# Optimization experiments

Hardware: AMD Instinct MI355X
Metric: run time of the kernel (lower is better)

The kernel has to match this reference:

```python
import jax, jax.numpy as jnp
import numpy as np

B, H, S, DK = 2, 8, 4096, 64


def setup_inputs() -> dict:
    key = jax.random.key(0)
    kq, kk, kv = jax.random.split(key, 3)
    queries = jax.random.normal(kq, (B, H, S, DK), dtype=jnp.float32)
    keys = jax.random.normal(kk, (B, H, S, DK), dtype=jnp.float32)
    values = jax.random.normal(kv, (B, H, S, DK), dtype=jnp.float32)
    # causal mask: 1.0 where attention is disallowed (strictly upper triangle)
    mask = jnp.triu(jnp.ones((S, S), dtype=jnp.float32), k=1)
    return {"queries": queries, "keys": keys, "values": values, "d_k": DK, "mask": mask}


def reference(queries, keys, values, d_k, mask):
    # scores: [B, H, S, S]
    scale = 1.0 / jnp.sqrt(jnp.float32(d_k))
    scores = jnp.einsum("bhqd,bhkd->bhqk", queries, keys) * scale
    if mask is not None:
        scores = scores + (-1e9) * mask  # broadcast [S,S] over [B,H,S,S]
    weights = jax.nn.softmax(scores, axis=-1)
    return jnp.einsum("bhqk,bhkd->bhqd", weights, values)
```

## Files before the change

### kernel.cpp

```cpp
#include <hip/hip_runtime.h>

typedef __bf16 bf16x8 __attribute__((ext_vector_type(8)));
typedef unsigned short u16x8 __attribute__((ext_vector_type(8)));
typedef unsigned short u16x4 __attribute__((ext_vector_type(4)));
typedef float f32x4 __attribute__((ext_vector_type(4)));

#define MFMA16(a, b, c) __builtin_amdgcn_mfma_f32_16x16x32_bf16((a), (b), (c), 0, 0, 0)

constexpr int SEQ  = 4096;
constexpr int DH   = 64;
constexpr int BH   = 16;
constexpr int LSTR = 72;
constexpr float SCALE_LOG2E = 0.125f * 1.44269504088896f;

__device__ __forceinline__ unsigned short f2bf(float f) {
  unsigned int u = __float_as_uint(f);
  u += 0x7fffu + ((u >> 16) & 1u);
  return (unsigned short)(u >> 16);
}

__global__ __launch_bounds__(256)
void prep_9990093930993(const float* __restrict__ K, const float* __restrict__ V,
                        unsigned short* __restrict__ Kb, unsigned short* __restrict__ Vtb) {
  const int tile = blockIdx.x, bh = blockIdx.y, tid = threadIdx.x;

  {
    const int row = tid >> 2;
    const int c0  = (tid & 3) * 16;
    const float* kr = K + (((long)bh * SEQ + tile * 64) + row) * DH + c0;
    float4 x0 = *(const float4*)(kr);
    float4 x1 = *(const float4*)(kr + 4);
    float4 x2 = *(const float4*)(kr + 8);
    float4 x3 = *(const float4*)(kr + 12);
    u16x8 a, b;
    a[0]=f2bf(x0.x); a[1]=f2bf(x0.y); a[2]=f2bf(x0.z); a[3]=f2bf(x0.w);
    a[4]=f2bf(x1.x); a[5]=f2bf(x1.y); a[6]=f2bf(x1.z); a[7]=f2bf(x1.w);
    b[0]=f2bf(x2.x); b[1]=f2bf(x2.y); b[2]=f2bf(x2.z); b[3]=f2bf(x2.w);
    b[4]=f2bf(x3.x); b[5]=f2bf(x3.y); b[6]=f2bf(x3.z); b[7]=f2bf(x3.w);
    unsigned short* ko = Kb + (((long)bh * SEQ + tile * 64) + row) * DH + c0;
    *(u16x8*)ko = a;
    *(u16x8*)(ko + 8) = b;
  }

  {
    const int d  = tid & 63;
    const int kg = tid >> 6;
    const float* vp = V + ((long)bh * SEQ + tile * 64) * DH;
    unsigned short* op = Vtb + (((long)bh * 64 + tile) * 64 + d) * 64 + kg * 16;
    #pragma unroll
    for (int h = 0; h < 2; ++h) {
      u16x8 o;
      #pragma unroll
      for (int j = 0; j < 8; ++j)
        o[j] = f2bf(vp[(kg * 16 + h * 8 + j) * DH + d]);
      *(u16x8*)(op + h * 8) = o;
    }
  }
}

__global__ __launch_bounds__(256, 2)
void attn6_9990093930993(const float* __restrict__ Qg,
                         const unsigned short* __restrict__ Kb,
                         const unsigned short* __restrict__ Vtb,
                         float* __restrict__ Og) {
  __shared__ unsigned short Kt[2][64 * LSTR];
  __shared__ unsigned short Vt[2][64 * LSTR];
  __shared__ unsigned short Pt[4][32 * LSTR];

  const int tid  = threadIdx.x;
  const int wave = tid >> 6;
  const int lane = tid & 63;
  const int l16  = lane & 15;
  const int lg   = lane >> 4;

  int s, bhi;
  {
    const int id = blockIdx.x;
    if (id < 256) { s = 31 - (id >> 4); bhi = id & 15; }
    else          { const int j = id - 256; s = j >> 4; bhi = j & 15; }
  }
  const long bh = bhi;
  const int  qt = 2 * s + 1;

  const float*          Qp = Qg  + bh * (long)(SEQ * DH);
  const unsigned short* Kp = Kb  + bh * (long)(SEQ * DH);
  const unsigned short* Vp = Vtb + bh * (long)(SEQ * DH);
  float*                Op = Og  + bh * (long)(SEQ * DH);

  const int qrow0 = s * 128 + wave * 32;

  const int srow = tid >> 2;
  const int scol = (tid & 3) * 16;
  const int f    = tid * 16;

  bf16x8 vone;
  {
    u16x8 t1;
    #pragma unroll
    for (int j = 0; j < 8; ++j) t1[j] = 0x3F80;
    vone = __builtin_bit_cast(bf16x8, t1);
  }

  bf16x8 qf[2][2];
  #pragma unroll
  for (int g = 0; g < 2; ++g) {
    const float* qr = Qp + (long)(qrow0 + g * 16 + l16) * DH + lg * 8;
    #pragma unroll
    for (int h = 0; h < 2; ++h) {
      float4 a = *(const float4*)(qr + h * 32);
      float4 b = *(const float4*)(qr + h * 32 + 4);
      u16x8 t2;
      t2[0] = f2bf(a.x * SCALE_LOG2E); t2[1] = f2bf(a.y * SCALE_LOG2E);
      t2[2] = f2bf(a.z * SCALE_LOG2E); t2[3] = f2bf(a.w * SCALE_LOG2E);
      t2[4] = f2bf(b.x * SCALE_LOG2E); t2[5] = f2bf(b.y * SCALE_LOG2E);
      t2[6] = f2bf(b.z * SCALE_LOG2E); t2[7] = f2bf(b.w * SCALE_LOG2E);
      qf[g][h] = __builtin_bit_cast(bf16x8, t2);
    }
  }
  const int qdiag0 = (qrow0) >> 6;
  const int qdiag1 = (qrow0 + 16) >> 6;

  f32x4 oacc0[4] = {}, oacc1[4] = {};
  f32x4 accl0 = {}, accl1 = {};

  u16x8 pk0, pk1, pv0, pv1;
  pk0 = *(const u16x8*)(Kp + f); pk1 = *(const u16x8*)(Kp + f + 8);
  pv0 = *(const u16x8*)(Vp + f); pv1 = *(const u16x8*)(Vp + f + 8);

  #pragma unroll 1
  for (int t = 0; t <= qt; ++t) {
    const int buf = t & 1;
    *(u16x8*)&Kt[buf][srow * LSTR + scol]     = pk0;
    *(u16x8*)&Kt[buf][srow * LSTR + scol + 8] = pk1;
    *(u16x8*)&Vt[buf][srow * LSTR + scol]     = pv0;
    *(u16x8*)&Vt[buf][srow * LSTR + scol + 8] = pv1;
    __syncthreads();

    if (t < qt) {
      const unsigned short* ks = Kp + (long)(t + 1) * 4096;
      const unsigned short* vs = Vp + (long)(t + 1) * 4096;
      pk0 = *(const u16x8*)(ks + f); pk1 = *(const u16x8*)(ks + f + 8);
      pv0 = *(const u16x8*)(vs + f); pv1 = *(const u16x8*)(vs + f + 8);
    }

    #pragma unroll
    for (int kt = 0; kt < 4; ++kt) {
      const bf16x8 kf0 = __builtin_bit_cast(bf16x8, *(const u16x8*)&Kt[buf][(kt*16 + l16) * LSTR + lg * 8]);
      const bf16x8 kf1 = __builtin_bit_cast(bf16x8, *(const u16x8*)&Kt[buf][(kt*16 + l16) * LSTR + 32 + lg * 8]);
      const int k0 = t * 64 + kt * 16 + lg * 4;
      #pragma unroll
      for (int g = 0; g < 2; ++g) {
        f32x4 st = {0.f, 0.f, 0.f, 0.f};
        st = MFMA16(kf0, qf[g][0], st);
        st = MFMA16(kf1, qf[g][1], st);
        if (t >= (g ? qdiag1 : qdiag0)) {
          const int qg = qrow0 + g * 16 + l16;
          #pragma unroll
          for (int r = 0; r < 4; ++r)
            if (k0 + r > qg) st[r] = -1e30f;
        }
        u16x4 w;
        w[0] = f2bf(__builtin_amdgcn_exp2f(st[0]));
        w[1] = f2bf(__builtin_amdgcn_exp2f(st[1]));
        w[2] = f2bf(__builtin_amdgcn_exp2f(st[2]));
        w[3] = f2bf(__builtin_amdgcn_exp2f(st[3]));
        *(u16x4*)&Pt[wave][(g * 16 + l16) * LSTR + kt * 16 + lg * 4] = w;
      }
    }

    #pragma unroll
    for (int ks2 = 0; ks2 < 2; ++ks2) {
      const bf16x8 pf0 = __builtin_bit_cast(bf16x8, *(const u16x8*)&Pt[wave][l16 * LSTR + ks2 * 32 + lg * 8]);
      const bf16x8 pf1 = __builtin_bit_cast(bf16x8, *(const u16x8*)&Pt[wave][(16 + l16) * LSTR + ks2 * 32 + lg * 8]);
      accl0 = MFMA16(pf0, vone, accl0);
      accl1 = MFMA16(pf1, vone, accl1);
      #pragma unroll
      for (int dt = 0; dt < 4; ++dt) {
        const bf16x8 vf = __builtin_bit_cast(bf16x8, *(const u16x8*)&Vt[buf][(dt*16 + l16) * LSTR + ks2 * 32 + lg * 8]);
        oacc0[dt] = MFMA16(pf0, vf, oacc0[dt]);
        oacc1[dt] = MFMA16(pf1, vf, oacc1[dt]);
      }
    }
  }

  #pragma unroll
  for (int r = 0; r < 4; ++r) {
    const float inv0 = 1.0f / accl0[r];
    const float inv1 = 1.0f / accl1[r];
    float* orow0 = Op + (long)(qrow0 + lg * 4 + r) * DH + l16;
    float* orow1 = Op + (long)(qrow0 + 16 + lg * 4 + r) * DH + l16;
    #pragma unroll
    for (int dt = 0; dt < 4; ++dt) {
      orow0[dt * 16] = oacc0[dt][r] * inv0;
      orow1[dt * 16] = oacc1[dt][r] * inv1;
    }
  }
}

__global__ __launch_bounds__(256, 2)
void attn_fwd_fb_9990093930993(const float* __restrict__ Qg, const float* __restrict__ Kg,
                               const float* __restrict__ Vg, float* __restrict__ Og) {
  constexpr int FSTR = 88;
  __shared__ unsigned short Kt[64 * FSTR];
  __shared__ unsigned short Vt[64 * FSTR];
  __shared__ unsigned short Pt[4][16 * FSTR];
  const int tid = threadIdx.x, wave = tid >> 6, lane = tid & 63;
  const int l16 = lane & 15, lg = lane >> 4;
  const int qtile = blockIdx.x; const long bh = blockIdx.y;
  const float* Qp = Qg + bh * (long)(SEQ * DH);
  const float* Kp = Kg + bh * (long)(SEQ * DH);
  const float* Vp = Vg + bh * (long)(SEQ * DH);
  float* Op = Og + bh * (long)(SEQ * DH);
  const int qrow0 = qtile * 64 + wave * 16;
  bf16x8 qf[2];
  {
    const float* qr = Qp + (long)(qrow0 + l16) * DH + lg * 8;
    #pragma unroll
    for (int s = 0; s < 2; ++s) {
      float4 a = *(const float4*)(qr + s * 32);
      float4 b = *(const float4*)(qr + s * 32 + 4);
      u16x8 t2;
      t2[0]=f2bf(a.x*0.125f); t2[1]=f2bf(a.y*0.125f); t2[2]=f2bf(a.z*0.125f); t2[3]=f2bf(a.w*0.125f);
      t2[4]=f2bf(b.x*0.125f); t2[5]=f2bf(b.y*0.125f); t2[6]=f2bf(b.z*0.125f); t2[7]=f2bf(b.w*0.125f);
      qf[s] = __builtin_bit_cast(bf16x8, t2);
    }
  }
  float m[4] = {-1e30f,-1e30f,-1e30f,-1e30f}, lsum[4] = {0,0,0,0};
  f32x4 oacc[4] = {};
  for (int t = 0; t <= qtile; ++t) {
    const int kvb = t * 64;
    #pragma unroll
    for (int j = 0; j < 4; ++j) {
      const int idx = j * 256 + tid, row = idx >> 4, c4 = (idx & 15) * 4;
      const long goff = (long)(kvb + row) * DH + c4;
      float4 kx = *(const float4*)(Kp + goff);
      float4 vx = *(const float4*)(Vp + goff);
      u16x4 kb; kb[0]=f2bf(kx.x); kb[1]=f2bf(kx.y); kb[2]=f2bf(kx.z); kb[3]=f2bf(kx.w);
      *(u16x4*)&Kt[row * FSTR + c4] = kb;
      Vt[(c4+0)*FSTR+row]=f2bf(vx.x); Vt[(c4+1)*FSTR+row]=f2bf(vx.y);
      Vt[(c4+2)*FSTR+row]=f2bf(vx.z); Vt[(c4+3)*FSTR+row]=f2bf(vx.w);
    }
    __syncthreads();
    float sv[16];
    #pragma unroll
    for (int kt = 0; kt < 4; ++kt) {
      bf16x8 kf0 = __builtin_bit_cast(bf16x8, *(const u16x8*)&Kt[(kt*16+l16)*FSTR + lg*8]);
      bf16x8 kf1 = __builtin_bit_cast(bf16x8, *(const u16x8*)&Kt[(kt*16+l16)*FSTR + 32 + lg*8]);
      f32x4 st = {0,0,0,0};
      st = MFMA16(qf[0], kf0, st); st = MFMA16(qf[1], kf1, st);
      const int kg = kvb + kt*16 + l16;
      #pragma unroll
      for (int r = 0; r < 4; ++r) {
        const int qg = qrow0 + lg*4 + r;
        sv[kt*4+r] = (kg > qg) ? -1e30f : st[r];
      }
    }
    float alpha[4], psum[4];
    #pragma unroll
    for (int r = 0; r < 4; ++r) {
      float rm = fmaxf(fmaxf(sv[r], sv[4+r]), fmaxf(sv[8+r], sv[12+r]));
      #pragma unroll
      for (int d = 1; d < 16; d <<= 1) rm = fmaxf(rm, __shfl_xor(rm, d));
      const float mn = fmaxf(m[r], rm);
      alpha[r] = __expf(m[r] - mn); m[r] = mn; psum[r] = 0.f;
    }
    #pragma unroll
    for (int kt = 0; kt < 4; ++kt)
      #pragma unroll
      for (int r = 0; r < 4; ++r) {
        const float p = __expf(sv[kt*4+r] - m[r]);
        psum[r] += p;
        Pt[wave][(lg*4+r)*FSTR + kt*16 + l16] = f2bf(p);
      }
    #pragma unroll
    for (int r = 0; r < 4; ++r) {
      float ps = psum[r];
      #pragma unroll
      for (int d = 1; d < 16; d <<= 1) ps += __shfl_xor(ps, d);
      lsum[r] = lsum[r] * alpha[r] + ps;
    }
    #pragma unroll
    for (int dt = 0; dt < 4; ++dt)
      #pragma unroll
      for (int r = 0; r < 4; ++r) oacc[dt][r] *= alpha[r];
    #pragma unroll
    for (int ks2 = 0; ks2 < 2; ++ks2) {
      bf16x8 pf = __builtin_bit_cast(bf16x8, *(const u16x8*)&Pt[wave][l16*FSTR + ks2*32 + lg*8]);
      #pragma unroll
      for (int dt = 0; dt < 4; ++dt) {
        bf16x8 vf = __builtin_bit_cast(bf16x8, *(const u16x8*)&Vt[(dt*16+l16)*FSTR + ks2*32 + lg*8]);
        oacc[dt] = MFMA16(pf, vf, oacc[dt]);
      }
    }
    __syncthreads();
  }
  #pragma unroll
  for (int r = 0; r < 4; ++r) {
    const float inv = 1.0f / lsum[r];
    float* orow = Op + (long)(qrow0 + lg*4 + r) * DH + l16;
    #pragma unroll
    for (int dt = 0; dt < 4; ++dt) orow[dt*16] = oacc[dt][r] * inv;
  }
}

extern "C" void kernel_launch(void* const* d_in, const int* in_sizes, int n_in,
                              void* d_out, int out_size, void* d_ws, size_t ws_size,
                              hipStream_t stream) {
  (void)in_sizes; (void)n_in; (void)out_size;
  const float* Q = (const float*)d_in[0];
  const float* K = (const float*)d_in[1];
  const float* V = (const float*)d_in[2];
  float* O = (float*)d_out;

  const size_t TSZ = (size_t)BH * SEQ * DH * sizeof(unsigned short);
  if (ws_size >= 2 * TSZ) {
    unsigned short* Kb  = (unsigned short*)d_ws;
    unsigned short* Vtb = Kb + (size_t)BH * SEQ * DH;
    prep_9990093930993<<<dim3(SEQ / 64, BH), dim3(256), 0, stream>>>(K, V, Kb, Vtb);
    attn6_9990093930993<<<dim3(512), dim3(256), 0, stream>>>(Q, Kb, Vtb, O);
  } else {
    attn_fwd_fb_9990093930993<<<dim3(SEQ / 64, BH), dim3(256), 0, stream>>>(Q, K, V, O);
  }
}
```

Baseline: 206.4 us.

## Single-buffer K/V LDS tiles, raise occupancy to 4 blocks, use hardware bf16 convert

Drops the double-buffered K/V shared-memory tiles in favour of a single buffer, adding a second barrier at the end of each iteration to protect reuse. With the LDS footprint reduced, launch bounds now request 4 blocks per CU instead of 2, relying on more resident waves to hide latency. The software round-to-nearest bf16 conversion for Q and the softmax weights is replaced by the compiler's native float-to-bf16 cast, which may lower to a hardware conversion instruction. The risks are the extra barrier per tile and register pressure from the higher occupancy target, and with only 512 blocks launched the extra occupancy may not be used.

Measured after the change: 201.6 us. 1.02x faster.

```diff
diff --git a/kernel.cpp b/kernel.cpp
--- a/kernel.cpp
+++ b/kernel.cpp
@@ -17,6 +17,10 @@
   unsigned int u = __float_as_uint(f);
   u += 0x7fffu + ((u >> 16) & 1u);
   return (unsigned short)(u >> 16);
+}
+
+__device__ __forceinline__ unsigned short f2bf_hw(float f) {
+  return __builtin_bit_cast(unsigned short, static_cast<__bf16>(f));
 }
 
 __global__ __launch_bounds__(256)
@@ -58,13 +62,13 @@
   }
 }
 
-__global__ __launch_bounds__(256, 2)
-void attn6_9990093930993(const float* __restrict__ Qg,
+__global__ __launch_bounds__(256, 4)
+void attn9_9990093930993(const float* __restrict__ Qg,
                          const unsigned short* __restrict__ Kb,
                          const unsigned short* __restrict__ Vtb,
                          float* __restrict__ Og) {
-  __shared__ unsigned short Kt[2][64 * LSTR];
-  __shared__ unsigned short Vt[2][64 * LSTR];
+  __shared__ unsigned short Kt[64 * LSTR];
+  __shared__ unsigned short Vt[64 * LSTR];
   __shared__ unsigned short Pt[4][32 * LSTR];
 
   const int tid  = threadIdx.x;
@@ -110,10 +114,10 @@
       float4 a = *(const float4*)(qr + h * 32);
       float4 b = *(const float4*)(qr + h * 32 + 4);
       u16x8 t2;
-      t2[0] = f2bf(a.x * SCALE_LOG2E); t2[1] = f2bf(a.y * SCALE_LOG2E);
-      t2[2] = f2bf(a.z * SCALE_LOG2E); t2[3] = f2bf(a.w * SCALE_LOG2E);
-      t2[4] = f2bf(b.x * SCALE_LOG2E); t2[5] = f2bf(b.y * SCALE_LOG2E);
-      t2[6] = f2bf(b.z * SCALE_LOG2E); t2[7] = f2bf(b.w * SCALE_LOG2E);
+      t2[0] = f2bf_hw(a.x * SCALE_LOG2E); t2[1] = f2bf_hw(a.y * SCALE_LOG2E);
+      t2[2] = f2bf_hw(a.z * SCALE_LOG2E); t2[3] = f2bf_hw(a.w * SCALE_LOG2E);
+      t2[4] = f2bf_hw(b.x * SCALE_LOG2E); t2[5] = f2bf_hw(b.y * SCALE_LOG2E);
+      t2[6] = f2bf_hw(b.z * SCALE_LOG2E); t2[7] = f2bf_hw(b.w * SCALE_LOG2E);
       qf[g][h] = __builtin_bit_cast(bf16x8, t2);
     }
   }
@@ -129,11 +133,10 @@
 
   #pragma unroll 1
   for (int t = 0; t <= qt; ++t) {
-    const int buf = t & 1;
-    *(u16x8*)&Kt[buf][srow * LSTR + scol]     = pk0;
-    *(u16x8*)&Kt[buf][srow * LSTR + scol + 8] = pk1;
-    *(u16x8*)&Vt[buf][srow * LSTR + scol]     = pv0;
-    *(u16x8*)&Vt[buf][srow * LSTR + scol + 8] = pv1;
+    *(u16x8*)&Kt[srow * LSTR + scol]     = pk0;
+    *(u16x8*)&Kt[srow * LSTR + scol + 8] = pk1;
+    *(u16x8*)&Vt[srow * LSTR + scol]     = pv0;
+    *(u16x8*)&Vt[srow * LSTR + scol + 8] = pv1;
     __syncthreads();
 
     if (t < qt) {
@@ -145,8 +148,8 @@
 
     #pragma unroll
     for (int kt = 0; kt < 4; ++kt) {
-      const bf16x8 kf0 = __builtin_bit_cast(bf16x8, *(const u16x8*)&Kt[buf][(kt*16 + l16) * LSTR + lg * 8]);
-      const bf16x8 kf1 = __builtin_bit_cast(bf16x8, *(const u16x8*)&Kt[buf][(kt*16 + l16) * LSTR + 32 + lg * 8]);
+      const bf16x8 kf0 = __builtin_bit_cast(bf16x8, *(const u16x8*)&Kt[(kt*16 + l16) * LSTR + lg * 8]);
+      const bf16x8 kf1 = __builtin_bit_cast(bf16x8, *(const u16x8*)&Kt[(kt*16 + l16) * LSTR + 32 + lg * 8]);
       const int k0 = t * 64 + kt * 16 + lg * 4;
       #pragma unroll
       for (int g = 0; g < 2; ++g) {
@@ -160,10 +163,10 @@
             if (k0 + r > qg) st[r] = -1e30f;
         }
         u16x4 w;
-        w[0] = f2bf(__builtin_amdgcn_exp2f(st[0]));
-        w[1] = f2bf(__builtin_amdgcn_exp2f(st[1]));
-        w[2] = f2bf(__builtin_amdgcn_exp2f(st[2]));
-        w[3] = f2bf(__builtin_amdgcn_exp2f(st[3]));
+        w[0] = f2bf_hw(__builtin_amdgcn_exp2f(st[0]));
+        w[1] = f2bf_hw(__builtin_amdgcn_exp2f(st[1]));
+        w[2] = f2bf_hw(__builtin_amdgcn_exp2f(st[2]));
+        w[3] = f2bf_hw(__builtin_amdgcn_exp2f(st[3]));
         *(u16x4*)&Pt[wave][(g * 16 + l16) * LSTR + kt * 16 + lg * 4] = w;
       }
     }
@@ -176,11 +179,12 @@
       accl1 = MFMA16(pf1, vone, accl1);
       #pragma unroll
       for (int dt = 0; dt < 4; ++dt) {
-        const bf16x8 vf = __builtin_bit_cast(bf16x8, *(const u16x8*)&Vt[buf][(dt*16 + l16) * LSTR + ks2 * 32 + lg * 8]);
+        const bf16x8 vf = __builtin_bit_cast(bf16x8, *(const u16x8*)&Vt[(dt*16 + l16) * LSTR + ks2 * 32 + lg * 8]);
         oacc0[dt] = MFMA16(pf0, vf, oacc0[dt]);
         oacc1[dt] = MFMA16(pf1, vf, oacc1[dt]);
       }
     }
+    __syncthreads();
   }
 
   #pragma unroll
@@ -317,7 +321,7 @@
     unsigned short* Kb  = (unsigned short*)d_ws;
     unsigned short* Vtb = Kb + (size_t)BH * SEQ * DH;
     prep_9990093930993<<<dim3(SEQ / 64, BH), dim3(256), 0, stream>>>(K, V, Kb, Vtb);
-    attn6_9990093930993<<<dim3(512), dim3(256), 0, stream>>>(Q, Kb, Vtb, O);
+    attn9_9990093930993<<<dim3(512), dim3(256), 0, stream>>>(Q, Kb, Vtb, O);
   } else {
     attn_fwd_fb_9990093930993<<<dim3(SEQ / 64, BH), dim3(256), 0, stream>>>(Q, K, V, O);
   }
```
